# Performance work log

Measured on AMD Instinct MI355X. Metric: run time of the kernel, lower is better.

The kernel has to match this reference:

```python
import jax, jax.numpy as jnp
import numpy as np

NEG = -1000000000.0

def _gru(x, h, W_ih, W_hh, b_ih, b_hh):
    # torch GRUCell semantics; W_ih: [3H, H_in], W_hh: [3H, H]
    gi = x @ W_ih.T + b_ih
    gh = h @ W_hh.T + b_hh
    i_r, i_z, i_n = jnp.split(gi, 3, axis=-1)
    h_r, h_z, h_n = jnp.split(gh, 3, axis=-1)
    r = jax.nn.sigmoid(i_r + h_r)
    z = jax.nn.sigmoid(i_z + h_z)
    n = jnp.tanh(i_n + r * h_n)
    return (1.0 - z) * n + z * h

def setup_inputs():
    key = jax.random.key(0)
    ks = jax.random.split(key, 32)
    N, E, ND, ED, H, P, L, M, S = 50000, 800000, 16, 16, 128, 16, 8, 6, 320
    sc = 0.05
    inp = {}
    inp['node_feat'] = jax.random.normal(ks[0], (N, ND), jnp.float32)
    inp['edge_feat'] = jax.random.normal(ks[1], (E, ED), jnp.float32)
    inp['edge_index'] = jax.random.randint(ks[2], (2, E), 0, N)
    inp['paths'] = jax.random.randint(ks[3], (P, L), 0, E)
    inp['path_mask'] = jnp.ones((P,), jnp.int32)
    inp['path_features'] = jax.random.normal(ks[4], (P, 3), jnp.float32)
    inp['mod_masks'] = jnp.ones((P, M), jnp.int32)
    inp['spec_masks'] = jnp.ones((P, M, S), jnp.int32)
    inp['path_spectrum'] = jax.random.uniform(ks[5], (P, S), jnp.float32)
    # parameters
    inp['W_np'] = jax.random.normal(ks[6], (ND, H), jnp.float32) * sc
    inp['b_np'] = jnp.zeros((H,), jnp.float32)
    inp['W_ep'] = jax.random.normal(ks[7], (ED, H), jnp.float32) * sc
    inp['b_ep'] = jnp.zeros((H,), jnp.float32)
    inp['W_msg'] = jax.random.normal(ks[8], (2 * H, H), jnp.float32) * sc
    inp['b_msg'] = jnp.zeros((H,), jnp.float32)
    inp['W_ih'] = jax.random.normal(ks[9], (3 * H, H), jnp.float32) * sc
    inp['b_ih'] = jnp.zeros((3 * H,), jnp.float32)
    inp['W_hh'] = jax.random.normal(ks[10], (3 * H, H), jnp.float32) * sc
    inp['b_hh'] = jnp.zeros((3 * H,), jnp.float32)
    inp['W_path'] = jax.random.normal(ks[11], (H, 1), jnp.float32) * sc
    inp['b_path'] = jnp.zeros((1,), jnp.float32)
    inp['W_mod'] = jax.random.normal(ks[12], (H + 3, M), jnp.float32) * sc
    inp['b_mod'] = jnp.zeros((M,), jnp.float32)
    inp['conv1_w'] = jax.random.normal(ks[13], (8, 1, 5), jnp.float32) * sc
    inp['conv1_b'] = jnp.zeros((8,), jnp.float32)
    inp['conv2_w'] = jax.random.normal(ks[14], (1, 8, 1), jnp.float32) * sc
    inp['conv2_b'] = jnp.zeros((1,), jnp.float32)
    inp['W_val'] = jax.random.normal(ks[15], (H, 1), jnp.float32) * sc
    inp['b_val'] = jnp.zeros((1,), jnp.float32)
    return inp

def reference(node_feat, edge_feat, edge_index, paths, path_mask, path_features,
              mod_masks, spec_masks, path_spectrum,
              W_np, b_np, W_ep, b_ep, W_msg, b_msg, W_ih, b_ih, W_hh, b_hh,
              W_path, b_path, W_mod, b_mod, conv1_w, conv1_b, conv2_w, conv2_b,
              W_val, b_val):
    N = node_feat.shape[0]
    # --- GNN encoder (3 iterations of gather -> message -> scatter -> GRU) ---
    h = node_feat @ W_np + b_np                       # [N, H]
    e = edge_feat @ W_ep + b_ep                       # [E, H]
    src, dst = edge_index[0], edge_index[1]
    for _ in range(3):
        m = jnp.concatenate([h[src], e], axis=-1) @ W_msg + b_msg   # [E, H]
        agg = jax.ops.segment_sum(m, dst, num_segments=N)           # index_add
        h = _gru(agg, h, W_ih, W_hh, b_ih, b_hh)
    # --- value head ---
    g = h.mean(axis=0)
    value = (g @ W_val + b_val).squeeze()
    # --- path agent (deterministic=True -> argmax) ---
    z = e[paths].mean(axis=1)                         # [P, H]
    logits_p = (z @ W_path + b_path).squeeze(-1)      # [P]
    logits_p = jnp.where(path_mask == 0, NEG, logits_p)
    p = jnp.argmax(logits_p)
    logp_p = jax.nn.log_softmax(logits_p)[p]
    z_p = z[p]
    # --- modulation agent ---
    x_m = jnp.concatenate([z_p, path_features[p]], axis=-1)
    logits_m = x_m @ W_mod + b_mod                    # [M]
    logits_m = jnp.where(mod_masks[p] == 0, NEG, logits_m)
    m_sel = jnp.argmax(logits_m)
    logp_m = jax.nn.log_softmax(logits_m)[m_sel]
    # --- spectrum agent ---
    spec = path_spectrum[p][None, None, :]            # [1,1,S]
    h1 = jax.nn.relu(jax.lax.conv_general_dilated(
        spec, conv1_w, (1,), [(2, 2)], dimension_numbers=('NCH', 'OIH', 'NCH'))
        + conv1_b[None, :, None])
    h2 = jax.lax.conv_general_dilated(
        h1, conv2_w, (1,), [(0, 0)], dimension_numbers=('NCH', 'OIH', 'NCH'))
    logits_f = h2.squeeze() + conv2_b[0]
    logits_f = jnp.where(spec_masks[p, m_sel] == 0, NEG, logits_f)
    f = jnp.argmax(logits_f)
    logp_f = jax.nn.log_softmax(logits_f)[f]
    logprob = logp_p + logp_m + logp_f
    return (p, f, m_sel, logprob, value)
```

## Files before the change

### kernel.cpp

```cpp
#include <hip/hip_runtime.h>
#include <hip/hip_bf16.h>
#include <math.h>

#define NN 50000
#define NE 800000
#define HD 128
#define FD 16
#define NPATH 16
#define PL 8
#define NM 6
#define NS 320
#define NSB 782
#define AK 320
#define AKU 160
#define AK1 64
#define EPB 2048
#define NBLK 391
#define NBKT 196
#define MBT 391
#define NEGV -1000000000.0f

typedef unsigned int uint;
typedef unsigned short ushort;
typedef short bf16x8 __attribute__((ext_vector_type(8)));
typedef float f32x4 __attribute__((ext_vector_type(4)));

__device__ __forceinline__ float frcp(float x){ return __builtin_amdgcn_rcpf(x); }
__device__ __forceinline__ float fsigm(float x){ return frcp(1.0f + __expf(-x)); }
__device__ __forceinline__ float ftanh(float x){ return 1.0f - 2.0f*frcp(__expf(2.0f*x) + 1.0f); }

__device__ __forceinline__ ushort f2b(float f){
    union { __hip_bfloat16 h; ushort u; } v;
    v.h = __float2bfloat16(f);
    return v.u;
}
__device__ __forceinline__ float b2f(ushort s){
    union{uint u; float f;} v; v.u = ((uint)s)<<16; return v.f;
}
__device__ __forceinline__ float blo(uint v){ return b2f((ushort)(v&0xFFFF)); }
__device__ __forceinline__ float bhi(uint v){ return b2f((ushort)(v>>16)); }
__device__ __forceinline__ uint pack2(float a, float b){ return (uint)f2b(a) | (((uint)f2b(b))<<16); }

__device__ __forceinline__ void gload16(const void* g, void* l){
    __builtin_amdgcn_global_load_lds(
        (const __attribute__((address_space(1))) unsigned int*)g,
        (__attribute__((address_space(3))) unsigned int*)l,
        16, 0, 0);
}

__global__ void k_hist(const int* __restrict__ ei, int* __restrict__ C){
    __shared__ int h[NBKT];
    int tid = threadIdx.x, blk = blockIdx.x;
    if (tid < NBKT) h[tid] = 0;
    __syncthreads();
    int e0 = blk*EPB;
    for (int i=tid; i<EPB; i+=256){
        int e = e0+i;
        if (e < NE) atomicAdd(&h[ei[NE+e]>>8], 1);
    }
    __syncthreads();
    if (tid < NBKT) C[blk*NBKT + tid] = h[tid];
}

__global__ void k_cscanA(int* __restrict__ C, int* __restrict__ bkttot){
    int b = blockIdx.x*4 + (threadIdx.x>>6);
    int lane = threadIdx.x & 63;
    if (b >= NBKT) return;
    int carry = 0;
    for (int c=0; c<7; ++c){
        int i = c*64 + lane;
        int v = (i<NBLK)? C[i*NBKT + b] : 0;
        int x = v;
        #pragma unroll
        for (int d=1; d<64; d<<=1){ int y = __shfl_up(x,d); if (lane>=d) x += y; }
        if (i<NBLK) C[i*NBKT + b] = carry + (x - v);
        carry += __shfl(x, 63);
    }
    if (lane==0) bkttot[b] = carry;
}

__global__ void k_bscan(const int* __restrict__ bkttot, int* __restrict__ bktbase,
                        int* __restrict__ offs){
    int tid = threadIdx.x, lane = tid&63, w = tid>>6;
    int v = (tid<NBKT)? bkttot[tid] : 0;
    int x = v;
    #pragma unroll
    for (int d=1; d<64; d<<=1){ int y = __shfl_up(x,d); if (lane>=d) x += y; }
    __shared__ int wsum[4];
    if (lane==63) wsum[w] = x;
    __syncthreads();
    int base = 0;
    #pragma unroll
    for (int j=0;j<4;j++) if (j<w) base += wsum[j];
    int excl = base + x - v;
    if (tid < NBKT) bktbase[tid] = excl;
    if (tid == NBKT){ bktbase[NBKT] = excl; offs[NN] = excl; }
}

__global__ void k_scatA(const int* __restrict__ ei, const int* __restrict__ C,
                        const int* __restrict__ bktbase, int2* __restrict__ bkt2){
    __shared__ int cur[NBKT];
    __shared__ int cbase[NBKT];
    int tid = threadIdx.x, blk = blockIdx.x;
    if (tid < NBKT){ cur[tid] = 0; cbase[tid] = bktbase[tid] + C[blk*NBKT + tid]; }
    __syncthreads();
    int e0 = blk*EPB;
    for (int i=tid; i<EPB; i+=256){
        int e = e0+i;
        if (e >= NE) break;
        int dst = ei[NE+e];
        int bkt = dst>>8;
        int r = atomicAdd(&cur[bkt], 1);
        bkt2[cbase[bkt] + r] = make_int2(dst, e);
    }
}

__global__ void k_scatB(const int* __restrict__ ei, const int2* __restrict__ bkt2,
                        const int* __restrict__ bktbase,
                        int* __restrict__ offs, int2* __restrict__ csr2){
    __shared__ int cnt[256];
    __shared__ int cur[256];
    __shared__ int wsum[4];
    int b = blockIdx.x, tid = threadIdx.x, lane = tid&63, w = tid>>6;
    int d0 = b<<8;
    cnt[tid] = 0;
    __syncthreads();
    int lo = bktbase[b], hi = bktbase[b+1];
    for (int i=lo+tid; i<hi; i+=256) atomicAdd(&cnt[bkt2[i].x & 255], 1);
    __syncthreads();
    int v = cnt[tid], x = v;
    #pragma unroll
    for (int d=1; d<64; d<<=1){ int y = __shfl_up(x,d); if (lane>=d) x += y; }
    if (lane==63) wsum[w] = x;
    __syncthreads();
    int base = 0;
    #pragma unroll
    for (int j=0;j<4;j++) if (j<w) base += wsum[j];
    int o = lo + base + x - v;
    if (d0+tid < NN) offs[d0+tid] = o;
    cur[tid] = o;
    __syncthreads();
    for (int i=lo+tid; i<hi; i+=256){
        int2 p = bkt2[i];
        int pos = atomicAdd(&cur[p.x & 255], 1);
        csr2[pos] = make_int2(ei[p.y], p.y);
    }
}

__global__ void k_gat16(const int2* __restrict__ csr2,
                        const float* __restrict__ edge_feat, const float* __restrict__ nf,
                        const int* __restrict__ offs,
                        float* __restrict__ ef_sum, float* __restrict__ nf_sum){
    int node = blockIdx.x*4 + (threadIdx.x>>6);
    int lane = threadIdx.x & 63;
    int k = lane & 15, sub = lane >> 4;
    int b = offs[node], e2 = offs[node+1];
    float ae = 0.f, an = 0.f;
    int i = b + sub;
    for (; i + 4 < e2; i += 8){
        int2 p0 = csr2[i], p1 = csr2[i+4];
        float f0 = edge_feat[(size_t)p0.y*FD + k];
        float g0 = nf[(size_t)p0.x*FD + k];
        float f1 = edge_feat[(size_t)p1.y*FD + k];
        float g1 = nf[(size_t)p1.x*FD + k];
        ae += f0 + f1; an += g0 + g1;
    }
    if (i < e2){
        int2 p0 = csr2[i];
        ae += edge_feat[(size_t)p0.y*FD + k];
        an += nf[(size_t)p0.x*FD + k];
    }
    ae += __shfl_xor(ae, 16); ae += __shfl_xor(ae, 32);
    an += __shfl_xor(an, 16); an += __shfl_xor(an, 32);
    if (sub == 0){ ef_sum[node*FD + k] = ae; nf_sum[node*FD + k] = an; }
}

__global__ void k_folds(const float* __restrict__ W_ep, const float* __restrict__ b_ep,
                        const float* __restrict__ W_msg, const float* __restrict__ b_msg,
                        float* __restrict__ Wf, float* __restrict__ bfv){
    int o = blockIdx.x*256 + threadIdx.x;
    if (o < FD*HD){
        int k=o>>7, c=o&127;
        float acc=0.f;
        for (int m=0;m<HD;m++) acc += W_ep[k*HD+m]*W_msg[(HD+m)*HD+c];
        Wf[o]=acc;
    } else if (o < FD*HD+HD){
        int c=o-FD*HD;
        float acc=b_msg[c];
        for (int m=0;m<HD;m++) acc += b_ep[m]*W_msg[(HD+m)*HD+c];
        bfv[c]=acc;
    }
}

__global__ void k_wprep2(const float* __restrict__ W_ih, const float* __restrict__ W_hh,
                         const float* __restrict__ W_msg, const float* __restrict__ Wf,
                         const float* __restrict__ bfv,
                         const float* __restrict__ b_ih, const float* __restrict__ b_hh,
                         ushort* __restrict__ W2T, float* __restrict__ Wt32){
    int c = blockIdx.x;
    int k = threadIdx.x;
    int j = c>>2, g = c&3;
    float v = 0.f;
    if (k < 128){
        float acc = 0.f;
        if (g < 3){
            const float* wm = W_msg + (size_t)k*HD;
            const float* wi = W_ih + (size_t)(g*HD+j)*HD;
            for (int m=0;m<HD;m++) acc += wm[m]*wi[m];
        }
        Wt32[(size_t)c*HD + k] = acc;
        v = acc;
    } else if (k < 256){
        int kk = k-128;
        if (g==0)      v = W_hh[(size_t)j*HD+kk];
        else if (g==1) v = W_hh[(size_t)(HD+j)*HD+kk];
        else if (g==3) v = W_hh[(size_t)(2*HD+j)*HD+kk];
    } else if (k < 272){
        if (g < 3){
            const float* wf = Wf + (size_t)(k-256)*HD;
            const float* wi = W_ih + (size_t)(g*HD+j)*HD;
            float acc=0.f;
            for (int m=0;m<HD;m++) acc += wf[m]*wi[m];
            v = acc;
        }
    } else if (k == 272){
        if (g < 3){
            const float* wi = W_ih + (size_t)(g*HD+j)*HD;
            float acc=0.f;
            for (int m=0;m<HD;m++) acc += bfv[m]*wi[m];
            v = acc;
        }
    } else if (k == 273){
        v = (g==0)? b_ih[j]+b_hh[j] : (g==1)? b_ih[HD+j]+b_hh[HD+j]
          : (g==2)? b_ih[2*HD+j] : b_hh[2*HD+j];
    }
    W2T[(size_t)c*AK + k] = f2b(v);
}

__global__ void k_wprep1(const float* __restrict__ W_np, const float* __restrict__ b_np,
                         const float* __restrict__ W_hh, const float* __restrict__ Wt32,
                         const ushort* __restrict__ W2T, ushort* __restrict__ W1T){
    int c = blockIdx.x;
    int k = threadIdx.x;
    int j = c>>2, g = c&3;
    float v = 0.f;
    if (k < 16){
        if (g != 2){
            int gp = (g==3)? 2 : g;
            const float* wh = W_hh + (size_t)(gp*HD + j)*HD;
            const float* wn = W_np + (size_t)k*HD;
            float acc=0.f;
            for (int m=0;m<HD;m++) acc += wn[m]*wh[m];
            v = acc;
        }
    } else if (k < 32){
        const float* wt = Wt32 + (size_t)c*HD;
        const float* wn = W_np + (size_t)(k-16)*HD;
        float acc=0.f;
        for (int m=0;m<HD;m++) acc += wn[m]*wt[m];
        v = acc;
    } else if (k < 48){
        v = b2f(W2T[(size_t)c*AK + 256 + (k-32)]);
    } else if (k == 48){
        float acc = b2f(W2T[(size_t)c*AK + 272]);
        const float* wt = Wt32 + (size_t)c*HD;
        for (int m=0;m<HD;m++) acc += b_np[m]*wt[m];
        v = acc;
    } else if (k == 49){
        float acc = b2f(W2T[(size_t)c*AK + 273]);
        if (g != 2){
            int gp = (g==3)? 2 : g;
            const float* wh = W_hh + (size_t)(gp*HD + j)*HD;
            for (int m=0;m<HD;m++) acc += b_np[m]*wh[m];
        }
        v = acc;
    }
    W1T[(size_t)c*AK1 + k] = f2b(v);
}

__global__ void k_prep2(const float* __restrict__ nf, const float* __restrict__ nf_sum,
                        const float* __restrict__ ef_sum, const int* __restrict__ offs,
                        ushort* __restrict__ A1p, ushort* __restrict__ A){
    int idx = blockIdx.x*256 + threadIdx.x;
    int n = idx>>5, c2 = idx&31;
    int k = c2*2, k1 = k+1;
    float d = (float)(offs[n+1] - offs[n]);
    float v0 = (k<16)? nf[n*FD+k] : (k<32)? nf_sum[n*FD+k-16] : (k<48)? ef_sum[n*FD+k-32]
             : (k==48)? d : 0.f;
    float v1 = (k1<16)? nf[n*FD+k1] : (k1<32)? nf_sum[n*FD+k1-16] : (k1<48)? ef_sum[n*FD+k1-32]
             : (k1==49)? 1.f : 0.f;
    ((uint*)A1p)[(size_t)n*32 + c2] = pack2(v0,v1);
    int col = 256 + k;
    float s0 = (col<272)? ef_sum[n*FD + col-256] : (col==272)? d : 0.f;
    float s1 = (col+1<272)? ef_sum[n*FD + col+1-256] : (col+1==273)? 1.f : 0.f;
    ((uint*)A)[(size_t)n*AKU + 128 + c2] = pack2(s0,s1);
}

template<bool IT1>
__global__ __launch_bounds__(256, 4) void k_fused(const ushort* __restrict__ Asrc,
                                                  const ushort* __restrict__ Bt,
                                                  const float* __restrict__ nf,
                                                  const float* __restrict__ W_np,
                                                  const float* __restrict__ b_np,
                                                  ushort* __restrict__ Ah){
    __shared__ __align__(16) short LDS[128*128];
    short* As = LDS;
    short* Bs = LDS + 128*64;
    const int bid = blockIdx.x;
    const int xcd = bid & 7;
    const int t = bid >> 3;
    const int gb = t & 3;
    const int mt = xcd + ((t >> 2) << 3);
    if (mt >= MBT) return;
    const int tid = threadIdx.x;
    const int lane = tid & 63, w = tid>>6;
    const int wm = w>>1, wn = w&1;
    const int n0 = gb*128, m0 = mt*128;
    const int jbase = n0>>2;
    const int AKA = IT1 ? AK1 : AK;
    const int rl  = lane>>3;
    const int sg  = (lane&7) ^ (rl&7);
    f32x4 acc[4][4] = {};
    const int nsteps = IT1 ? 1 : 5;
    for (int kk=0; kk<nsteps; ++kk){
        __syncthreads();
        #pragma unroll
        for (int i=0;i<4;i++){
            int cc = w*4 + i;
            int rowl = (cc<<3) + rl;
            int ar = m0 + rowl; if (ar >= NN) ar = NN-1;
            gload16(Asrc + (size_t)ar*AKA + kk*64 + sg*8, As + cc*512);
            gload16(Bt + (size_t)(n0+rowl)*AKA + kk*64 + sg*8, Bs + cc*512);
        }
        __syncthreads();
        #pragma unroll
        for (int ksel=0; ksel<2; ++ksel){
            bf16x8 af[4], bfr[4];
            #pragma unroll
            for (int t2=0;t2<4;t2++){
                int arow = wm*64 + t2*16 + (lane&15);
                int aslot = (ksel*4 + (lane>>4)) ^ (arow&7);
                af[t2] = *(const bf16x8*)&As[arow*64 + aslot*8];
                int brow = wn*64 + t2*16 + (lane&15);
                int bslot = (ksel*4 + (lane>>4)) ^ (brow&7);
                bfr[t2] = *(const bf16x8*)&Bs[brow*64 + bslot*8];
            }
            #pragma unroll
            for (int mi=0;mi<4;mi++)
                #pragma unroll
                for (int ni=0;ni<4;ni++)
                    acc[mi][ni] = __builtin_amdgcn_mfma_f32_16x16x32_bf16(af[mi], bfr[ni], acc[mi][ni], 0,0,0);
        }
    }
    __syncthreads();
    #pragma unroll
    for (int mi=0;mi<4;mi++){
        #pragma unroll
        for (int ni=0;ni<4;ni++){
            #pragma unroll
            for (int r=0;r<4;r++){
                int row = wm*64 + mi*16 + (lane>>4)*4 + r;
                int col = wn*64 + ni*16 + (lane&15);
                int pc = (col&3) | (((col>>2) ^ (row&7))<<2);
                LDS[row*128 + pc] = (short)f2b(acc[mi][ni][r]);
            }
        }
    }
    __syncthreads();
    {
        int jp = tid&15, rg = tid>>4;
        int jg = jbase + jp*2;
        #pragma unroll
        for (int rr=0; rr<8; ++rr){
            int row = rg*8 + rr;
            int n = m0 + row;
            if (n >= NN) continue;
            uint2 g0 = *(const uint2*)&LDS[row*128 + (((jp*2)   ^ (row&7))<<2)];
            uint2 g1 = *(const uint2*)&LDS[row*128 + (((jp*2+1) ^ (row&7))<<2)];
            float ha, hb;
            if constexpr (IT1){
                const float* x = nf + (size_t)n*FD;
                float a = b_np[jg], b = b_np[jg+1];
                #pragma unroll
                for (int k=0;k<FD;k++){
                    float xv = x[k];
                    a += xv*W_np[k*HD + jg];
                    b += xv*W_np[k*HD + jg + 1];
                }
                ha = a; hb = b;
            } else {
                uint vh = ((const uint*)Ah)[(size_t)n*AKU + 64 + (n0>>3) + jp];
                ha = blo(vh); hb = bhi(vh);
            }
            float r0 = fsigm(blo(g0.x)), z0 = fsigm(bhi(g0.x));
            float nn0 = ftanh(blo(g0.y) + r0*bhi(g0.y));
            float r1 = fsigm(blo(g1.x)), z1 = fsigm(bhi(g1.x));
            float nn1 = ftanh(blo(g1.y) + r1*bhi(g1.y));
            float h0 = (1.f-z0)*nn0 + z0*ha;
            float h1 = (1.f-z1)*nn1 + z1*hb;
            ((uint*)Ah)[(size_t)n*AKU + 64 + (n0>>3) + jp] = pack2(h0,h1);
        }
    }
}

__global__ void k_gather(ushort* __restrict__ A, const int* __restrict__ offs,
                         const int2* __restrict__ csr2){
    int node = blockIdx.x*4 + (threadIdx.x>>6);
    int c2 = threadIdx.x & 63;
    int b = offs[node], e2 = offs[node+1];
    float a0 = 0.f, a1 = 0.f;
    const uint* hp = (const uint*)A;
    int i = b;
    for (; i + 8 <= e2; i += 8){
        int s0=csr2[i].x,  s1=csr2[i+1].x, s2=csr2[i+2].x, s3=csr2[i+3].x;
        int s4=csr2[i+4].x,s5=csr2[i+5].x, s6=csr2[i+6].x, s7=csr2[i+7].x;
        uint v0=hp[(size_t)s0*AKU+64+c2], v1=hp[(size_t)s1*AKU+64+c2],
             v2=hp[(size_t)s2*AKU+64+c2], v3=hp[(size_t)s3*AKU+64+c2],
             v4=hp[(size_t)s4*AKU+64+c2], v5=hp[(size_t)s5*AKU+64+c2],
             v6=hp[(size_t)s6*AKU+64+c2], v7=hp[(size_t)s7*AKU+64+c2];
        a0 += blo(v0)+blo(v1)+blo(v2)+blo(v3)+blo(v4)+blo(v5)+blo(v6)+blo(v7);
        a1 += bhi(v0)+bhi(v1)+bhi(v2)+bhi(v3)+bhi(v4)+bhi(v5)+bhi(v6)+bhi(v7);
    }
    if (i + 4 <= e2){
        int s0=csr2[i].x,s1=csr2[i+1].x,s2=csr2[i+2].x,s3=csr2[i+3].x;
        uint v0=hp[(size_t)s0*AKU+64+c2], v1=hp[(size_t)s1*AKU+64+c2],
             v2=hp[(size_t)s2*AKU+64+c2], v3=hp[(size_t)s3*AKU+64+c2];
        a0 += blo(v0)+blo(v1)+blo(v2)+blo(v3);
        a1 += bhi(v0)+bhi(v1)+bhi(v2)+bhi(v3);
        i += 4;
    }
    for (; i < e2; ++i){
        uint v = hp[(size_t)csr2[i].x*AKU+64+c2];
        a0 += blo(v); a1 += bhi(v);
    }
    ((uint*)A)[(size_t)node*AKU + c2] = pack2(a0,a1);
}

__global__ void k_sum1(const ushort* __restrict__ A, float* __restrict__ partial){
    int bid = blockIdx.x, tid = threadIdx.x;
    int lane = tid&63, w2 = tid>>6;
    int nb = bid*64;
    float a0=0.f, a1=0.f;
    const uint* hp = (const uint*)A;
    #pragma unroll
    for (int r=w2; r<64; r+=4){
        int n = nb + r;
        if (n < NN){
            uint v = hp[(size_t)n*AKU + 64 + lane];
            a0 += blo(v); a1 += bhi(v);
        }
    }
    __shared__ float s0[4][64], s1[4][64];
    s0[w2][lane]=a0; s1[w2][lane]=a1;
    __syncthreads();
    if (w2==0){
        a0 = s0[0][lane]+s0[1][lane]+s0[2][lane]+s0[3][lane];
        a1 = s1[0][lane]+s1[1][lane]+s1[2][lane]+s1[3][lane];
        ((float2*)partial)[(size_t)bid*64 + lane] = make_float2(a0,a1);
    }
}
__global__ void k_sum2(const float* __restrict__ partial, float* __restrict__ gsum){
    int c = blockIdx.x;
    int tid = threadIdx.x;
    int lane = tid&63, w = tid>>6;
    float a = 0.f;
    for (int b=tid; b<NSB; b+=256) a += partial[(size_t)b*128 + c];
    #pragma unroll
    for (int d=1; d<64; d<<=1) a += __shfl_xor(a, d);
    __shared__ float sh[4];
    if (lane==0) sh[w]=a;
    __syncthreads();
    if (tid==0) gsum[c] = sh[0]+sh[1]+sh[2]+sh[3];
}

__global__ void k_small(const float* __restrict__ ef, const int* __restrict__ paths,
                        const int* __restrict__ pmask, const float* __restrict__ pfeat,
                        const int* __restrict__ mmask, const int* __restrict__ smask,
                        const float* __restrict__ pspec,
                        const float* __restrict__ W_ep, const float* __restrict__ b_ep,
                        const float* __restrict__ W_path, const float* __restrict__ b_path,
                        const float* __restrict__ W_mod, const float* __restrict__ b_mod,
                        const float* __restrict__ c1w, const float* __restrict__ c1b,
                        const float* __restrict__ c2w, const float* __restrict__ c2b,
                        const float* __restrict__ W_val, const float* __restrict__ b_val,
                        const float* __restrict__ gsum, float* __restrict__ out){
    __shared__ float Wep_s[FD][HD];
    __shared__ float esum[NPATH][FD];
    __shared__ float z[NPATH][HD];
    __shared__ float lf[NS];
    __shared__ float spec[NS];
    __shared__ float red[8];
    __shared__ float scal[3];
    __shared__ int   sel[3];
    __shared__ float maxsh;
    int tid = threadIdx.x, lane = tid&63, w = tid>>6;

    for (int i=tid; i<FD*HD; i+=512) Wep_s[i>>7][i&127] = W_ep[i];
    if (tid < NPATH*FD){
        int p = tid>>4, k = tid&15;
        float a = 0.f;
        #pragma unroll
        for (int l=0;l<PL;l++){
            int eid = paths[p*PL + l];
            a += ef[(size_t)eid*FD + k];
        }
        esum[p][k] = a*0.125f;
    }
    __syncthreads();
    #pragma unroll
    for (int i=tid; i<NPATH*HD; i+=512){
        int p = i>>7, c = i&127;
        float a = b_ep[c];
        #pragma unroll
        for (int k=0;k<FD;k++) a += esum[p][k]*Wep_s[k][c];
        z[p][c] = a;
    }
    __syncthreads();
    {
        int p = tid>>5, sub = tid&31;
        float part = 0.f;
        #pragma unroll
        for (int c=sub;c<HD;c+=32) part += z[p][c]*W_path[c];
        #pragma unroll
        for (int d=16; d>=1; d>>=1) part += __shfl_xor(part, d);
        if (sub==0) lf[p] = (pmask[p]==0)? NEGV : part + b_path[0];
    }
    __syncthreads();
    if (w==0){
        float v = (lane<NPATH)? lf[lane] : -3.0e38f;
        float m = v;
        #pragma unroll
        for (int d=1; d<64; d<<=1) m = fmaxf(m, __shfl_xor(m, d));
        float e = (lane<NPATH)? __expf(v-m) : 0.f;
        #pragma unroll
        for (int d=1; d<64; d<<=1) e += __shfl_xor(e, d);
        int idx = (lane<NPATH && v==m)? lane : (1<<30);
        #pragma unroll
        for (int d=1; d<64; d<<=1) idx = min(idx, __shfl_xor(idx, d));
        if (lane==0){ sel[0]=idx; scal[0] = -logf(e); }
    }
    __syncthreads();
    int pstar = sel[0];
    if (w < NM){
        float part = 0.f;
        #pragma unroll
        for (int c=lane;c<HD;c+=64) part += z[pstar][c]*W_mod[c*NM + w];
        if (lane<3) part += pfeat[pstar*3+lane]*W_mod[(HD+lane)*NM + w];
        #pragma unroll
        for (int d=1; d<64; d<<=1) part += __shfl_xor(part, d);
        if (lane==0) red[w] = (mmask[pstar*NM + w]==0)? NEGV : part + b_mod[w];
    } else if (w == 7){
        float part = gsum[lane]*W_val[lane] + gsum[lane+64]*W_val[lane+64];
        #pragma unroll
        for (int d=1; d<64; d<<=1) part += __shfl_xor(part, d);
        if (lane==0) scal[2] = part/(float)NN + b_val[0];
    }
    __syncthreads();
    if (w==0){
        float v = (lane<NM)? red[lane] : -3.0e38f;
        float m = v;
        #pragma unroll
        for (int d=1; d<64; d<<=1) m = fmaxf(m, __shfl_xor(m, d));
        float e = (lane<NM)? __expf(v-m) : 0.f;
        #pragma unroll
        for (int d=1; d<64; d<<=1) e += __shfl_xor(e, d);
        int idx = (lane<NM && v==m)? lane : (1<<30);
        #pragma unroll
        for (int d=1; d<64; d<<=1) idx = min(idx, __shfl_xor(idx, d));
        if (lane==0){ sel[1]=idx; scal[1] = -logf(e); }
    }
    __syncthreads();
    int mstar = sel[1];
    if (tid < NS) spec[tid] = pspec[pstar*NS + tid];
    __syncthreads();
    float v = -3.0e38f;
    if (tid < NS){
        float acc = c2b[0];
        #pragma unroll
        for (int ch=0; ch<8; ch++){
            float a = c1b[ch];
            #pragma unroll
            for (int k=0;k<5;k++){
                int ss = tid + k - 2;
                if (ss>=0 && ss<NS) a += spec[ss]*c1w[ch*5+k];
            }
            a = fmaxf(a, 0.f);
            acc += a*c2w[ch];
        }
        v = (smask[pstar*NM*NS + mstar*NS + tid]==0) ? NEGV : acc;
    }
    float m = v;
    #pragma unroll
    for (int d=1; d<64; d<<=1) m = fmaxf(m, __shfl_xor(m, d));
    if (lane==0) red[w] = m;
    __syncthreads();
    if (tid==0){
        float mm = red[0];
        #pragma unroll
        for (int i=1;i<8;i++) mm = fmaxf(mm, red[i]);
        maxsh = mm; sel[2] = 1<<30;
    }
    __syncthreads();
    float M2 = maxsh;
    if (tid<NS && v==M2) atomicMin(&sel[2], tid);
    float e = (tid<NS)? __expf(v-M2) : 0.f;
    #pragma unroll
    for (int d=1; d<64; d<<=1) e += __shfl_xor(e, d);
    if (lane==0) red[w] = e;
    __syncthreads();
    if (tid==0){
        float se = 0.f;
        #pragma unroll
        for (int i=0;i<8;i++) se += red[i];
        out[0] = (float)pstar;
        out[1] = (float)sel[2];
        out[2] = (float)mstar;
        out[3] = scal[0] + scal[1] - logf(se);
        out[4] = scal[2];
    }
}

extern "C" void kernel_launch(void* const* d_in, const int* in_sizes, int n_in,
                              void* d_out, int out_size, void* d_ws, size_t ws_size,
                              hipStream_t stream) {
    (void)in_sizes; (void)n_in; (void)out_size; (void)ws_size;
    const float* node_feat     = (const float*)d_in[0];
    const float* edge_feat     = (const float*)d_in[1];
    const int*   edge_index    = (const int*)d_in[2];
    const int*   paths         = (const int*)d_in[3];
    const int*   path_mask     = (const int*)d_in[4];
    const float* path_features = (const float*)d_in[5];
    const int*   mod_masks     = (const int*)d_in[6];
    const int*   spec_masks    = (const int*)d_in[7];
    const float* path_spectrum = (const float*)d_in[8];
    const float* W_np  = (const float*)d_in[9];
    const float* b_np  = (const float*)d_in[10];
    const float* W_ep  = (const float*)d_in[11];
    const float* b_ep  = (const float*)d_in[12];
    const float* W_msg = (const float*)d_in[13];
    const float* b_msg = (const float*)d_in[14];
    const float* W_ih  = (const float*)d_in[15];
    const float* b_ih  = (const float*)d_in[16];
    const float* W_hh  = (const float*)d_in[17];
    const float* b_hh  = (const float*)d_in[18];
    const float* W_path = (const float*)d_in[19];
    const float* b_path = (const float*)d_in[20];
    const float* W_mod  = (const float*)d_in[21];
    const float* b_mod  = (const float*)d_in[22];
    const float* c1w = (const float*)d_in[23];
    const float* c1b = (const float*)d_in[24];
    const float* c2w = (const float*)d_in[25];
    const float* c2b = (const float*)d_in[26];
    const float* W_val = (const float*)d_in[27];
    const float* b_val = (const float*)d_in[28];

    char* ws = (char*)d_ws;
    size_t off = 0;
    auto alloc = [&](size_t bytes)->char*{
        char* p = ws + off;
        off += (bytes + 255) & ~(size_t)255;
        return p;
    };
    int*    offs    = (int*)alloc((size_t)(NN+1)*4);
    int*    Cmat    = (int*)alloc((size_t)NBLK*NBKT*4);
    int*    bkttot  = (int*)alloc((size_t)NBKT*4);
    int*    bktbase = (int*)alloc((size_t)(NBKT+1)*4);
    int2*   bkt2    = (int2*)alloc((size_t)NE*8);
    int2*   csr2    = (int2*)alloc((size_t)NE*8);
    float*  ef_sum  = (float*)alloc((size_t)NN*FD*4);
    float*  nf_sum  = (float*)alloc((size_t)NN*FD*4);
    float*  Wf      = (float*)alloc((size_t)FD*HD*4);
    float*  bfv     = (float*)alloc((size_t)HD*4);
    ushort* W2T     = (ushort*)alloc((size_t)512*AK*2);
    float*  Wt32    = (float*)alloc((size_t)512*HD*4);
    ushort* W1T     = (ushort*)alloc((size_t)512*AK1*2);
    ushort* A       = (ushort*)alloc((size_t)NN*AK*2);
    ushort* A1p     = (ushort*)alloc((size_t)NN*AK1*2);
    float*  partial = (float*)alloc((size_t)NSB*HD*4);
    float*  gsum    = (float*)alloc((size_t)HD*4);

    k_hist<<<NBLK, 256, 0, stream>>>(edge_index, Cmat);
    k_cscanA<<<(NBKT+3)/4, 256, 0, stream>>>(Cmat, bkttot);
    k_bscan<<<1, 256, 0, stream>>>(bkttot, bktbase, offs);
    k_scatA<<<NBLK, 256, 0, stream>>>(edge_index, Cmat, bktbase, bkt2);
    k_scatB<<<NBKT, 256, 0, stream>>>(edge_index, bkt2, bktbase, offs, csr2);
    k_gat16<<<NN/4, 256, 0, stream>>>(csr2, edge_feat, node_feat, offs, ef_sum, nf_sum);
    k_folds<<<9, 256, 0, stream>>>(W_ep, b_ep, W_msg, b_msg, Wf, bfv);
    k_wprep2<<<512, AK, 0, stream>>>(W_ih, W_hh, W_msg, Wf, bfv, b_ih, b_hh, W2T, Wt32);
    k_wprep1<<<512, AK1, 0, stream>>>(W_np, b_np, W_hh, Wt32, W2T, W1T);
    k_prep2<<<NN*32/256, 256, 0, stream>>>(node_feat, nf_sum, ef_sum, offs, A1p, A);

    const int GRID = 8*4*49;
    k_fused<true><<<GRID, 256, 0, stream>>>(A1p, W1T, node_feat, W_np, b_np, A);
    k_gather<<<NN/4, 256, 0, stream>>>(A, offs, csr2);
    k_fused<false><<<GRID, 256, 0, stream>>>(A, W2T, node_feat, W_np, b_np, A);
    k_gather<<<NN/4, 256, 0, stream>>>(A, offs, csr2);
    k_fused<false><<<GRID, 256, 0, stream>>>(A, W2T, node_feat, W_np, b_np, A);

    k_sum1<<<NSB, 256, 0, stream>>>(A, partial);
    k_sum2<<<HD, 256, 0, stream>>>(partial, gsum);
    k_small<<<1, 512, 0, stream>>>(edge_feat, paths, path_mask, path_features,
                                   mod_masks, spec_masks, path_spectrum,
                                   W_ep, b_ep, W_path, b_path, W_mod, b_mod,
                                   c1w, c1b, c2w, c2b, W_val, b_val,
                                   gsum, (float*)d_out);
}
```

Measured before the change: 269.2 us.

## Widen fused GRU GEMM tile to 256 cols and double-buffer hidden state

```diff
diff --git a/kernel.cpp b/kernel.cpp
--- a/kernel.cpp
+++ b/kernel.cpp
@@ -12,7 +12,9 @@
 #define NS 320
 #define NSB 782
 #define AK 320
-#define AKU 160
+#define A2S 192
+#define A2U 96
+#define HU 64
 #define AK1 64
 #define EPB 2048
 #define NBLK 391
@@ -280,7 +282,7 @@
 
 __global__ void k_prep2(const float* __restrict__ nf, const float* __restrict__ nf_sum,
                         const float* __restrict__ ef_sum, const int* __restrict__ offs,
-                        ushort* __restrict__ A1p, ushort* __restrict__ A){
+                        ushort* __restrict__ A1p, ushort* __restrict__ A2){
     int idx = blockIdx.x*256 + threadIdx.x;
     int n = idx>>5, c2 = idx&31;
     int k = c2*2, k1 = k+1;
@@ -290,47 +292,59 @@
     float v1 = (k1<16)? nf[n*FD+k1] : (k1<32)? nf_sum[n*FD+k1-16] : (k1<48)? ef_sum[n*FD+k1-32]
              : (k1==49)? 1.f : 0.f;
     ((uint*)A1p)[(size_t)n*32 + c2] = pack2(v0,v1);
-    int col = 256 + k;
-    float s0 = (col<272)? ef_sum[n*FD + col-256] : (col==272)? d : 0.f;
-    float s1 = (col+1<272)? ef_sum[n*FD + col+1-256] : (col+1==273)? 1.f : 0.f;
-    ((uint*)A)[(size_t)n*AKU + 128 + c2] = pack2(s0,s1);
+    int s = k;
+    float s0 = (s<16)? ef_sum[n*FD + s] : (s==16)? d : 0.f;
+    float s1 = (s+1<16)? ef_sum[n*FD + s+1] : (s+1==17)? 1.f : 0.f;
+    ((uint*)A2)[(size_t)n*A2U + 64 + c2] = pack2(s0,s1);
 }
 
 template<bool IT1>
-__global__ __launch_bounds__(256, 4) void k_fused(const ushort* __restrict__ Asrc,
+__global__ __launch_bounds__(512, 4) void k_fused(const ushort* __restrict__ Asrc,
                                                   const ushort* __restrict__ Bt,
+                                                  const ushort* __restrict__ Hp,
                                                   const float* __restrict__ nf,
                                                   const float* __restrict__ W_np,
                                                   const float* __restrict__ b_np,
-                                                  ushort* __restrict__ Ah){
-    __shared__ __align__(16) short LDS[128*128];
+                                                  ushort* __restrict__ Hn){
+    __shared__ __align__(16) short LDS[128*64 + 256*64];
     short* As = LDS;
     short* Bs = LDS + 128*64;
     const int bid = blockIdx.x;
     const int xcd = bid & 7;
     const int t = bid >> 3;
-    const int gb = t & 3;
-    const int mt = xcd + ((t >> 2) << 3);
+    const int npair = t & 1;
+    const int mt = xcd + ((t >> 1) << 3);
     if (mt >= MBT) return;
     const int tid = threadIdx.x;
     const int lane = tid & 63, w = tid>>6;
-    const int wm = w>>1, wn = w&1;
-    const int n0 = gb*128, m0 = mt*128;
-    const int jbase = n0>>2;
-    const int AKA = IT1 ? AK1 : AK;
+    const int wm = w>>2, wn = w&3;
+    const int n0 = npair*256, m0 = mt*128;
     const int rl  = lane>>3;
-    const int sg  = (lane&7) ^ (rl&7);
+    const int sg  = (lane&7) ^ rl;
     f32x4 acc[4][4] = {};
     const int nsteps = IT1 ? 1 : 5;
     for (int kk=0; kk<nsteps; ++kk){
         __syncthreads();
         #pragma unroll
-        for (int i=0;i<4;i++){
-            int cc = w*4 + i;
-            int rowl = (cc<<3) + rl;
-            int ar = m0 + rowl; if (ar >= NN) ar = NN-1;
-            gload16(Asrc + (size_t)ar*AKA + kk*64 + sg*8, As + cc*512);
-            gload16(Bt + (size_t)(n0+rowl)*AKA + kk*64 + sg*8, Bs + cc*512);
+        for (int i=0;i<6;i++){
+            int idx = w*6 + i;
+            if (idx < 16){
+                int rowl = (idx<<3) + rl;
+                int ar = m0 + rowl; if (ar >= NN) ar = NN-1;
+                const ushort* ap;
+                if constexpr (IT1) ap = Asrc + (size_t)ar*AK1 + sg*8;
+                else {
+                    if (kk < 2)      ap = Asrc + (size_t)ar*A2S + kk*64 + sg*8;
+                    else if (kk < 4) ap = Hp   + (size_t)ar*HD  + (kk-2)*64 + sg*8;
+                    else             ap = Asrc + (size_t)ar*A2S + 128 + sg*8;
+                }
+                gload16(ap, As + idx*512);
+            } else {
+                int bi = idx - 16;
+                int rowl = (bi<<3) + rl;
+                const int AKB = IT1 ? AK1 : AK;
+                gload16(Bt + (size_t)(n0+rowl)*AKB + kk*64 + sg*8, Bs + bi*512);
+            }
         }
         __syncthreads();
         #pragma unroll
@@ -352,101 +366,108 @@
                     acc[mi][ni] = __builtin_amdgcn_mfma_f32_16x16x32_bf16(af[mi], bfr[ni], acc[mi][ni], 0,0,0);
         }
     }
-    __syncthreads();
-    #pragma unroll
-    for (int mi=0;mi<4;mi++){
-        #pragma unroll
-        for (int ni=0;ni<4;ni++){
+    #pragma unroll
+    for (int h=0; h<2; ++h){
+        __syncthreads();
+        if ((wn>>1) == h){
+            int cw = wn & 1;
             #pragma unroll
-            for (int r=0;r<4;r++){
-                int row = wm*64 + mi*16 + (lane>>4)*4 + r;
-                int col = wn*64 + ni*16 + (lane&15);
-                int pc = (col&3) | (((col>>2) ^ (row&7))<<2);
-                LDS[row*128 + pc] = (short)f2b(acc[mi][ni][r]);
+            for (int mi=0;mi<4;mi++){
+                #pragma unroll
+                for (int ni=0;ni<4;ni++){
+                    #pragma unroll
+                    for (int r=0;r<4;r++){
+                        int row = wm*64 + mi*16 + (lane>>4)*4 + r;
+                        int col = cw*64 + ni*16 + (lane&15);
+                        int pc = (col&3) | (((col>>2) ^ (row&7))<<2);
+                        LDS[row*128 + pc] = (short)f2b(acc[mi][ni][r]);
+                    }
+                }
             }
         }
-    }
-    __syncthreads();
-    {
-        int jp = tid&15, rg = tid>>4;
-        int jg = jbase + jp*2;
-        #pragma unroll
-        for (int rr=0; rr<8; ++rr){
-            int row = rg*8 + rr;
-            int n = m0 + row;
-            if (n >= NN) continue;
-            uint2 g0 = *(const uint2*)&LDS[row*128 + (((jp*2)   ^ (row&7))<<2)];
-            uint2 g1 = *(const uint2*)&LDS[row*128 + (((jp*2+1) ^ (row&7))<<2)];
-            float ha, hb;
-            if constexpr (IT1){
-                const float* x = nf + (size_t)n*FD;
-                float a = b_np[jg], b = b_np[jg+1];
-                #pragma unroll
-                for (int k=0;k<FD;k++){
-                    float xv = x[k];
-                    a += xv*W_np[k*HD + jg];
-                    b += xv*W_np[k*HD + jg + 1];
+        __syncthreads();
+        {
+            int jp = tid&15, rg = tid>>4;
+            int jg = npair*128 + h*64 + jp*2;
+            int hoff = npair*32 + h*16 + jp;
+            #pragma unroll
+            for (int rr=0; rr<4; ++rr){
+                int row = rg*4 + rr;
+                int n = m0 + row;
+                if (n >= NN) continue;
+                uint2 g0 = *(const uint2*)&LDS[row*128 + (((jp*2)   ^ (row&7))<<2)];
+                uint2 g1 = *(const uint2*)&LDS[row*128 + (((jp*2+1) ^ (row&7))<<2)];
+                float ha, hb;
+                if constexpr (IT1){
+                    const float* x = nf + (size_t)n*FD;
+                    float a = b_np[jg], b = b_np[jg+1];
+                    #pragma unroll
+                    for (int k=0;k<FD;k++){
+                        float xv = x[k];
+                        a += xv*W_np[k*HD + jg];
+                        b += xv*W_np[k*HD + jg + 1];
+                    }
+                    ha = a; hb = b;
+                } else {
+                    uint vh = ((const uint*)Hp)[(size_t)n*HU + hoff];
+                    ha = blo(vh); hb = bhi(vh);
                 }
-                ha = a; hb = b;
-            } else {
-                uint vh = ((const uint*)Ah)[(size_t)n*AKU + 64 + (n0>>3) + jp];
-                ha = blo(vh); hb = bhi(vh);
+                float r0 = fsigm(blo(g0.x)), z0 = fsigm(bhi(g0.x));
+                float nn0 = ftanh(blo(g0.y) + r0*bhi(g0.y));
+                float r1 = fsigm(blo(g1.x)), z1 = fsigm(bhi(g1.x));
+                float nn1 = ftanh(blo(g1.y) + r1*bhi(g1.y));
+                float h0 = (1.f-z0)*nn0 + z0*ha;
+                float h1 = (1.f-z1)*nn1 + z1*hb;
+                ((uint*)Hn)[(size_t)n*HU + hoff] = pack2(h0,h1);
             }
-            float r0 = fsigm(blo(g0.x)), z0 = fsigm(bhi(g0.x));
-            float nn0 = ftanh(blo(g0.y) + r0*bhi(g0.y));
-            float r1 = fsigm(blo(g1.x)), z1 = fsigm(bhi(g1.x));
-            float nn1 = ftanh(blo(g1.y) + r1*bhi(g1.y));
-            float h0 = (1.f-z0)*nn0 + z0*ha;
-            float h1 = (1.f-z1)*nn1 + z1*hb;
-            ((uint*)Ah)[(size_t)n*AKU + 64 + (n0>>3) + jp] = pack2(h0,h1);
-        }
-    }
-}
-
-__global__ void k_gather(ushort* __restrict__ A, const int* __restrict__ offs,
-                         const int2* __restrict__ csr2){
+        }
+    }
+}
+
+__global__ void k_gather(ushort* __restrict__ A2, const int* __restrict__ offs,
+                         const int2* __restrict__ csr2, const ushort* __restrict__ H){
     int node = blockIdx.x*4 + (threadIdx.x>>6);
     int c2 = threadIdx.x & 63;
     int b = offs[node], e2 = offs[node+1];
     float a0 = 0.f, a1 = 0.f;
-    const uint* hp = (const uint*)A;
+    const uint* hp = (const uint*)H;
     int i = b;
     for (; i + 8 <= e2; i += 8){
         int s0=csr2[i].x,  s1=csr2[i+1].x, s2=csr2[i+2].x, s3=csr2[i+3].x;
         int s4=csr2[i+4].x,s5=csr2[i+5].x, s6=csr2[i+6].x, s7=csr2[i+7].x;
-        uint v0=hp[(size_t)s0*AKU+64+c2], v1=hp[(size_t)s1*AKU+64+c2],
-             v2=hp[(size_t)s2*AKU+64+c2], v3=hp[(size_t)s3*AKU+64+c2],
-             v4=hp[(size_t)s4*AKU+64+c2], v5=hp[(size_t)s5*AKU+64+c2],
-             v6=hp[(size_t)s6*AKU+64+c2], v7=hp[(size_t)s7*AKU+64+c2];
+        uint v0=hp[(size_t)s0*HU+c2], v1=hp[(size_t)s1*HU+c2],
+             v2=hp[(size_t)s2*HU+c2], v3=hp[(size_t)s3*HU+c2],
+             v4=hp[(size_t)s4*HU+c2], v5=hp[(size_t)s5*HU+c2],
+             v6=hp[(size_t)s6*HU+c2], v7=hp[(size_t)s7*HU+c2];
         a0 += blo(v0)+blo(v1)+blo(v2)+blo(v3)+blo(v4)+blo(v5)+blo(v6)+blo(v7);
         a1 += bhi(v0)+bhi(v1)+bhi(v2)+bhi(v3)+bhi(v4)+bhi(v5)+bhi(v6)+bhi(v7);
     }
     if (i + 4 <= e2){
         int s0=csr2[i].x,s1=csr2[i+1].x,s2=csr2[i+2].x,s3=csr2[i+3].x;
-        uint v0=hp[(size_t)s0*AKU+64+c2], v1=hp[(size_t)s1*AKU+64+c2],
-             v2=hp[(size_t)s2*AKU+64+c2], v3=hp[(size_t)s3*AKU+64+c2];
+        uint v0=hp[(size_t)s0*HU+c2], v1=hp[(size_t)s1*HU+c2],
+             v2=hp[(size_t)s2*HU+c2], v3=hp[(size_t)s3*HU+c2];
         a0 += blo(v0)+blo(v1)+blo(v2)+blo(v3);
         a1 += bhi(v0)+bhi(v1)+bhi(v2)+bhi(v3);
         i += 4;
     }
     for (; i < e2; ++i){
-        uint v = hp[(size_t)csr2[i].x*AKU+64+c2];
+        uint v = hp[(size_t)csr2[i].x*HU+c2];
         a0 += blo(v); a1 += bhi(v);
     }
-    ((uint*)A)[(size_t)node*AKU + c2] = pack2(a0,a1);
-}
-
-__global__ void k_sum1(const ushort* __restrict__ A, float* __restrict__ partial){
+    ((uint*)A2)[(size_t)node*A2U + c2] = pack2(a0,a1);
+}
+
+__global__ void k_sum1(const ushort* __restrict__ H, float* __restrict__ partial){
     int bid = blockIdx.x, tid = threadIdx.x;
     int lane = tid&63, w2 = tid>>6;
     int nb = bid*64;
     float a0=0.f, a1=0.f;
-    const uint* hp = (const uint*)A;
+    const uint* hp = (const uint*)H;
     #pragma unroll
     for (int r=w2; r<64; r+=4){
         int n = nb + r;
         if (n < NN){
-            uint v = hp[(size_t)n*AKU + 64 + lane];
+            uint v = hp[(size_t)n*HU + lane];
             a0 += blo(v); a1 += bhi(v);
         }
     }
@@ -674,8 +695,10 @@
     ushort* W2T     = (ushort*)alloc((size_t)512*AK*2);
     float*  Wt32    = (float*)alloc((size_t)512*HD*4);
     ushort* W1T     = (ushort*)alloc((size_t)512*AK1*2);
-    ushort* A       = (ushort*)alloc((size_t)NN*AK*2);
+    ushort* A2      = (ushort*)alloc((size_t)NN*A2S*2);
     ushort* A1p     = (ushort*)alloc((size_t)NN*AK1*2);
+    ushort* H0      = (ushort*)alloc((size_t)NN*HD*2);
+    ushort* H1      = (ushort*)alloc((size_t)NN*HD*2);
     float*  partial = (float*)alloc((size_t)NSB*HD*4);
     float*  gsum    = (float*)alloc((size_t)HD*4);
 
@@ -688,16 +711,16 @@
     k_folds<<<9, 256, 0, stream>>>(W_ep, b_ep, W_msg, b_msg, Wf, bfv);
     k_wprep2<<<512, AK, 0, stream>>>(W_ih, W_hh, W_msg, Wf, bfv, b_ih, b_hh, W2T, Wt32);
     k_wprep1<<<512, AK1, 0, stream>>>(W_np, b_np, W_hh, Wt32, W2T, W1T);
-    k_prep2<<<NN*32/256, 256, 0, stream>>>(node_feat, nf_sum, ef_sum, offs, A1p, A);
-
-    const int GRID = 8*4*49;
-    k_fused<true><<<GRID, 256, 0, stream>>>(A1p, W1T, node_feat, W_np, b_np, A);
-    k_gather<<<NN/4, 256, 0, stream>>>(A, offs, csr2);
-    k_fused<false><<<GRID, 256, 0, stream>>>(A, W2T, node_feat, W_np, b_np, A);
-    k_gather<<<NN/4, 256, 0, stream>>>(A, offs, csr2);
-    k_fused<false><<<GRID, 256, 0, stream>>>(A, W2T, node_feat, W_np, b_np, A);
-
-    k_sum1<<<NSB, 256, 0, stream>>>(A, partial);
+    k_prep2<<<NN*32/256, 256, 0, stream>>>(node_feat, nf_sum, ef_sum, offs, A1p, A2);
+
+    const int GRID = 8*2*49;
+    k_fused<true><<<GRID, 512, 0, stream>>>(A1p, W1T, H0, node_feat, W_np, b_np, H0);
+    k_gather<<<NN/4, 256, 0, stream>>>(A2, offs, csr2, H0);
+    k_fused<false><<<GRID, 512, 0, stream>>>(A2, W2T, H0, node_feat, W_np, b_np, H1);
+    k_gather<<<NN/4, 256, 0, stream>>>(A2, offs, csr2, H1);
+    k_fused<false><<<GRID, 512, 0, stream>>>(A2, W2T, H1, node_feat, W_np, b_np, H0);
+
+    k_sum1<<<NSB, 256, 0, stream>>>(H0, partial);
     k_sum2<<<HD, 256, 0, stream>>>(partial, gsum);
     k_small<<<1, 512, 0, stream>>>(edge_feat, paths, path_mask, path_features,
                                    mod_masks, spec_masks, path_spectrum,
```

Result: slower. 320.9 us (+19.2%).
